# Performance work log

Hardware: AMD Instinct MI355X
Metric: run time of the kernel (lower is better)

Reference implementation:

```python
import jax, jax.numpy as jnp
import numpy as np

D = 256; H = 8; DH = D // H; FF = 1024; L = 2048; M = 1024


def _mlp(x, w0, b0, w1, b1, w2, b2):
    # 3-layer MLP, relu on all but last (matches MLP class)
    x = jax.nn.relu(x @ w0 + b0)
    x = jax.nn.relu(x @ w1 + b1)
    return x @ w2 + b2


def _ln(x, g, b, eps=1e-5):
    m = jnp.mean(x, axis=-1, keepdims=True)
    v = jnp.var(x, axis=-1, keepdims=True)
    return (x - m) * jax.lax.rsqrt(v + eps) * g + b


def setup_inputs():
    key = jax.random.key(0)
    ks = jax.random.split(key, 16)
    p = lambda i, shape: jax.random.normal(ks[i], shape, jnp.float32) * 0.02
    z = lambda *s: jnp.zeros(s, jnp.float32)
    o = lambda *s: jnp.ones(s, jnp.float32)
    # positions: ego covers [0, L), agent covers [L-M, 2L-M) -> exactly M shared positions
    return {
        'ego_q': jax.random.normal(ks[0], (1, L, D), jnp.float32),
        'agent_q': jax.random.normal(ks[1], (1, L, D), jnp.float32),
        'ego_pos': jnp.arange(L, dtype=jnp.int32),
        'agent_pos': jnp.arange(L, dtype=jnp.int32) + (L - M),
        'n_match': M,
        'fw0': p(2, (2 * D, D)), 'fb0': z(D),
        'fw1': p(3, (D, D)), 'fb1': z(D),
        'fw2': p(4, (D, D)), 'fb2': z(D),
        'wq': p(5, (D, D)), 'bq': z(D),
        'wk': p(6, (D, D)), 'bk': z(D),
        'wv': p(7, (D, D)), 'bv': z(D),
        'wo': p(8, (D, D)), 'bo': z(D),
        'g1': o(D), 'be1': z(D),
        'l1w': p(9, (D, FF)), 'l1b': z(FF),
        'l2w': p(10, (FF, D)), 'l2b': z(D),
        'g2': o(D), 'be2': z(D),
    }


def reference(ego_q, agent_q, ego_pos, agent_pos, n_match,
              fw0, fb0, fw1, fb1, fw2, fb2,
              wq, bq, wk, bk, wv, bv, wo, bo,
              g1, be1, l1w, l1b, l2w, l2b, g2, be2):
    La = agent_pos.shape[0]
    # vectorized replacement of the per-position dict/loop grouping:
    # for each ego position, find a matching agent position (positions sorted+unique)
    idx = jnp.clip(jnp.searchsorted(agent_pos, ego_pos), 0, La - 1)
    matched = (agent_pos[idx] == ego_pos)                     # (L,)
    pair = jnp.concatenate([ego_q, agent_q[:, idx, :]], axis=-1)  # (1, L, 2D)
    fused = _mlp(pair, fw0, fb0, fw1, fb1, fw2, fb2)          # (1, L, D)
    ego_out = jnp.where(matched[None, :, None], fused, ego_q)
    # agent queries whose positions are NOT in ego's set: indices [n_match, La)
    q = jnp.concatenate([ego_out, agent_q[:, n_match:, :]], axis=1)  # (1, 2L-M, D)
    kv = jnp.concatenate([ego_q, agent_q], axis=1)                   # (1, 2L, D)
    # MultiheadAttention (batch_first, eval mode -> no dropout)
    qh = (q @ wq + bq).reshape(1, -1, H, DH)
    kh = (kv @ wk + bk).reshape(1, -1, H, DH)
    vh = (kv @ wv + bv).reshape(1, -1, H, DH)
    scores = jnp.einsum('bqhd,bkhd->bhqk', qh, kh) * (1.0 / np.sqrt(DH))
    attn = jax.nn.softmax(scores, axis=-1)
    o = jnp.einsum('bhqk,bkhd->bqhd', attn, vh).reshape(1, -1, D) @ wo + bo
    x = _ln(q + o, g1, be1)
    ff = jax.nn.relu(x @ l1w + l1b) @ l2w + l2b
    return _ln(x + ff, g2, be2)
```

## Files before the change

kernel.cpp:

```cpp
#include <hip/hip_runtime.h>
#include <hip/hip_bf16.h>

typedef __hip_bfloat16 bf16;
typedef __bf16 bf16x8 __attribute__((ext_vector_type(8)));
typedef float  f32x16 __attribute__((ext_vector_type(16)));

__device__ __forceinline__ bool is_bf16_flag(const unsigned* g1w) {
    return *g1w == 0x3F803F80u;
}

__device__ __forceinline__ unsigned cvt_pk_bf16(float lo, float hi) {
    unsigned w;
    asm("v_cvt_pk_bf16_f32 %0, %1, %2" : "=v"(w) : "v"(lo), "v"(hi));
    return w;
}
__device__ __forceinline__ void permlane32_swap(unsigned& a, unsigned& b) {
    asm("v_permlane32_swap_b32 %0, %1" : "+v"(a), "+v"(b));
}

union FragU { unsigned u[4]; uint4 q; bf16x8 v; };

__device__ __forceinline__ float loadf(const void* p, size_t i, bool isb) {
    return isb ? __bfloat162float(((const bf16*)p)[i]) : ((const float*)p)[i];
}

__device__ __forceinline__ float4 load4rt(const void* p, size_t i, bool isb) {
    if (isb) {
        uint2 u = *(const uint2*)((const bf16*)p + i);
        float4 f;
        f.x = __uint_as_float(u.x << 16);
        f.y = __uint_as_float(u.x & 0xFFFF0000u);
        f.z = __uint_as_float(u.y << 16);
        f.w = __uint_as_float(u.y & 0xFFFF0000u);
        return f;
    }
    return *(const float4*)((const float*)p + i);
}

__device__ __forceinline__ void store4b(bf16* p, float4 v) {
    uint2 w;
    w.x = cvt_pk_bf16(v.x, v.y);
    w.y = cvt_pk_bf16(v.z, v.w);
    *(uint2*)p = w;
}

__device__ __forceinline__ float4 load4b(const bf16* p) {
    uint2 u = *(const uint2*)p;
    float4 f;
    f.x = __uint_as_float(u.x << 16);
    f.y = __uint_as_float(u.x & 0xFFFF0000u);
    f.z = __uint_as_float(u.y << 16);
    f.w = __uint_as_float(u.y & 0xFFFF0000u);
    return f;
}

#define NCVT 13
struct CvtArgs {
    const void* src[NCVT];
    float*      dst[NCVT];
    float       scale[NCVT];
    int         n4[NCVT];
    int         blk_end[NCVT];
};

__global__ void convert_all_kernel(CvtArgs a, const unsigned* __restrict__ g1w) {
    bool isb = is_bf16_flag(g1w);
    int b = blockIdx.x;
    int t = 0;
    while (b >= a.blk_end[t]) t++;
    int base = (t == 0) ? 0 : a.blk_end[t - 1];
    int i = (b - base) * 256 + threadIdx.x;
    if (i >= a.n4[t]) return;
    float sc = a.scale[t];
    float4 r = load4rt(a.src[t], (size_t)i * 4, isb);
    r.x *= sc; r.y *= sc; r.z *= sc; r.w *= sc;
    ((float4*)a.dst[t])[i] = r;
}

#define NWT 9
struct WtArgs {
    const void* src[NWT];
    bf16*       dst[NWT];
    int         K[NWT];
    int         N[NWT];
    float       scale[NWT];
    int         blk_end[NWT];
};

__global__ void wtrans_kernel(WtArgs a, const unsigned* __restrict__ g1w) {
    bool isb = is_bf16_flag(g1w);
    int b = blockIdx.x;
    int w = 0;
    while (b >= a.blk_end[w]) w++;
    int base = (w == 0) ? 0 : a.blk_end[w - 1];
    int tt = b - base;
    int tn = a.N[w] >> 6;
    int kr = (tt / tn) * 64, nc = (tt % tn) * 64;
    int N = a.N[w], K = a.K[w];
    float sc = a.scale[w];
    const void* src = a.src[w];
    __shared__ float ld[64][65];
    int t = threadIdx.x;
#pragma unroll
    for (int i = 0; i < 16; i++) {
        int f = t + i * 256;
        int r = f >> 6, c = f & 63;
        ld[r][c] = loadf(src, (size_t)(kr + r) * N + nc + c, isb) * sc;
    }
    __syncthreads();
    bf16* dst = a.dst[w];
#pragma unroll
    for (int i = 0; i < 16; i++) {
        int f = t + i * 256;
        int c = f >> 6, r = f & 63;
        dst[(size_t)(nc + c) * K + kr + r] = __float2bfloat16(ld[r][c]);
    }
}

__global__ void build_pair_kernel(const void* __restrict__ ego, const void* __restrict__ agent,
                                  const int* __restrict__ epos, const int* __restrict__ apos,
                                  int La, bf16* __restrict__ pair, int* __restrict__ mflag,
                                  const unsigned* __restrict__ g1w) {
    bool isb = is_bf16_flag(g1w);
    int t = threadIdx.x;
    int rb = t >> 7;
    int row = blockIdx.x * 2 + rb;
    int cc = (t & 127) * 4;
    __shared__ int s_idx[2];
    if ((t & 127) == 0) {
        int p = epos[row];
        int lo = 0, hi = La;
        while (lo < hi) { int mid = (lo + hi) >> 1; if (apos[mid] < p) lo = mid + 1; else hi = mid; }
        int idx = lo < La - 1 ? lo : La - 1;
        s_idx[rb] = idx;
        mflag[row] = (apos[idx] == p) ? 1 : 0;
    }
    __syncthreads();
    int idx = s_idx[rb];
    float4 v = (cc < 256) ? load4rt(ego, (size_t)row * 256 + cc, isb)
                          : load4rt(agent, (size_t)idx * 256 + (cc - 256), isb);
    store4b(pair + (size_t)row * 512 + cc, v);
}

template<int RELU>
__launch_bounds__(256)
__global__ void gemm_bf16_kernel(const bf16* __restrict__ A, const bf16* __restrict__ Bt,
                                 const float* __restrict__ bias, bf16* __restrict__ C,
                                 int M, int N, int K, int lda, int ldb, int ldc) {
    __shared__ __align__(16) char sA[64 * 128];
    __shared__ __align__(16) char sB[64 * 128];
    const int z = blockIdx.z;
    A += (size_t)z * K;
    Bt += (size_t)z * K;
    C += (size_t)z * M * ldc;

    const int t = threadIdx.x;
    const int lane = t & 63, wave = t >> 6;
    const int hi = lane >> 5, ql = lane & 31;
    const int bm = blockIdx.y * 64, bn = blockIdx.x * 64;
    const int wm = (wave & 1) * 32, wn = (wave >> 1) * 32;

    const int r0 = t >> 3, ch0 = t & 7;
    const int r1 = 32 + r0;
    const int wb0 = (r0 * 128 + ch0 * 16) ^ ((r0 & 7) << 4);
    const int wb1 = (r1 * 128 + ch0 * 16) ^ ((r1 & 7) << 4);

    uint4 ra0, ra1, rb0, rb1;
    {
        ra0 = *(const uint4*)&A [(size_t)(bm + r0) * lda + ch0 * 8];
        ra1 = *(const uint4*)&A [(size_t)(bm + r1) * lda + ch0 * 8];
        rb0 = *(const uint4*)&Bt[(size_t)(bn + r0) * ldb + ch0 * 8];
        rb1 = *(const uint4*)&Bt[(size_t)(bn + r1) * ldb + ch0 * 8];
    }

    f32x16 acc = {};
    const int swzA = ((wm + ql) & 7) << 4;
    const int swzB = ((wn + ql) & 7) << 4;
    const int rowA = (wm + ql) * 128;
    const int rowB = (wn + ql) * 128;

    for (int k0 = 0; k0 < K; k0 += 64) {
        __syncthreads();
        *(uint4*)(sA + wb0) = ra0;
        *(uint4*)(sA + wb1) = ra1;
        *(uint4*)(sB + wb0) = rb0;
        *(uint4*)(sB + wb1) = rb1;
        if (k0 + 64 < K) {
            int kn = k0 + 64;
            ra0 = *(const uint4*)&A [(size_t)(bm + r0) * lda + kn + ch0 * 8];
            ra1 = *(const uint4*)&A [(size_t)(bm + r1) * lda + kn + ch0 * 8];
            rb0 = *(const uint4*)&Bt[(size_t)(bn + r0) * ldb + kn + ch0 * 8];
            rb1 = *(const uint4*)&Bt[(size_t)(bn + r1) * ldb + kn + ch0 * 8];
        }
        __syncthreads();
#pragma unroll
        for (int kc = 0; kc < 4; kc++) {
            FragU af, bf_;
            af.q  = *(const uint4*)(sA + ((rowA + kc * 32 + hi * 16) ^ swzA));
            bf_.q = *(const uint4*)(sB + ((rowB + kc * 32 + hi * 16) ^ swzB));
            acc = __builtin_amdgcn_mfma_f32_32x32x16_bf16(af.v, bf_.v, acc, 0, 0, 0);
        }
    }

    int gn = bn + wn + ql;
    float bsv = (z == 0) ? bias[gn] : 0.f;
#pragma unroll
    for (int r = 0; r < 16; r++) {
        int mrow = (r & 3) + 8 * (r >> 2) + 4 * hi;
        float v = acc[r] + bsv;
        if (RELU) v = fmaxf(v, 0.f);
        C[(size_t)(bm + wm + mrow) * ldc + gn] = __float2bfloat16(v);
    }
}

__global__ void build_qkv_kernel(const void* __restrict__ ego, const void* __restrict__ agent,
                                 const bf16* __restrict__ fused, const int* __restrict__ mflag,
                                 int L, int Mm, int Nq, int Nk,
                                 bf16* __restrict__ qb, bf16* __restrict__ kvb,
                                 const unsigned* __restrict__ g1w) {
    bool isb = is_bf16_flag(g1w);
    int wave = threadIdx.x >> 6, lane = threadIdx.x & 63;
    int r = blockIdx.x * 4 + wave;
    int col = lane * 4;
    float4 kvv = (r < L) ? load4rt(ego, (size_t)r * 256 + col, isb)
                         : load4rt(agent, (size_t)(r - L) * 256 + col, isb);
    store4b(kvb + (size_t)r * 256 + col, kvv);
    if (r < Nq) {
        float4 qv;
        if (r < L) qv = mflag[r] ? load4b(fused + (size_t)r * 256 + col)
                                 : load4rt(ego, (size_t)r * 256 + col, isb);
        else       qv = load4rt(agent, (size_t)(Mm + r - L) * 256 + col, isb);
        store4b(qb + (size_t)r * 256 + col, qv);
    }
}

#define SPLITS 4

__launch_bounds__(256)
__global__ void attn_mfma_kernel(const bf16* __restrict__ qh,
                                 const bf16* __restrict__ kvh,
                                 float* __restrict__ pm, float* __restrict__ pl,
                                 bf16* __restrict__ pacc,
                                 int Nq, int Nk) {
    __shared__ __align__(16) char sK[64 * 128];
    __shared__ __align__(16) char sV[32 * 128];

    const int h = blockIdx.y, z = blockIdx.z;
    const int t = threadIdx.x;
    const int wave = t >> 6, lane = t & 63;
    const int ql = lane & 31, hi = lane >> 5;
    const int qbase = blockIdx.x * 128 + wave * 32;
    const int kbeg = z * (Nk / SPLITS);
    const int nkk = Nk / SPLITS;

    FragU qf0, qf1;
    {
        const bf16* qp = qh + (size_t)(qbase + ql) * 256 + h * 32;
        qf0.q = *(const uint4*)(qp + hi * 8);
        qf1.q = *(const uint4*)(qp + 16 + hi * 8);
    }

    float mrun = -1e30f, lrun = 0.f;
    f32x16 acc = {};

    const int skey = t >> 2, sch = t & 3;
    const int kwb = (skey * 128 + sch * 16) ^ ((skey & 7) << 4);

    uint4 rk = *(const uint4*)(kvh + (size_t)(kbeg + skey) * 512 + h * 32 + sch * 8);
    uint4 rv = *(const uint4*)(kvh + (size_t)(kbeg + lane) * 512 + 256 + h * 32 + wave * 8);

#pragma unroll 1
    for (int t0 = 0; t0 < nkk; t0 += 64) {
        __syncthreads();
        *(uint4*)(sK + kwb) = rk;
        {
            unsigned short sv[8] = {
                (unsigned short)(rv.x), (unsigned short)(rv.x >> 16),
                (unsigned short)(rv.y), (unsigned short)(rv.y >> 16),
                (unsigned short)(rv.z), (unsigned short)(rv.z >> 16),
                (unsigned short)(rv.w), (unsigned short)(rv.w >> 16)};
#pragma unroll
            for (int i = 0; i < 8; i++) {
                int dh = wave * 8 + i;
                *(unsigned short*)(sV + dh * 128 + ((lane * 2) ^ (i << 4))) = sv[i];
            }
        }
        if (t0 + 64 < nkk) {
            rk = *(const uint4*)(kvh + (size_t)(kbeg + t0 + 64 + skey) * 512 + h * 32 + sch * 8);
            rv = *(const uint4*)(kvh + (size_t)(kbeg + t0 + 64 + lane) * 512 + 256 + h * 32 + wave * 8);
        }
        __syncthreads();

        FragU ka, kb;
        f32x16 s0 = {}, s1 = {};
        {
            int row0 = ql, row1 = 32 + ql;
            int swz = (ql & 7) << 4;
            ka.q = *(const uint4*)(sK + ((row0 * 128 + hi * 16) ^ swz));
            s0 = __builtin_amdgcn_mfma_f32_32x32x16_bf16(ka.v, qf0.v, s0, 0, 0, 0);
            ka.q = *(const uint4*)(sK + ((row0 * 128 + 32 + hi * 16) ^ swz));
            s0 = __builtin_amdgcn_mfma_f32_32x32x16_bf16(ka.v, qf1.v, s0, 0, 0, 0);
            kb.q = *(const uint4*)(sK + ((row1 * 128 + hi * 16) ^ swz));
            s1 = __builtin_amdgcn_mfma_f32_32x32x16_bf16(kb.v, qf0.v, s1, 0, 0, 0);
            kb.q = *(const uint4*)(sK + ((row1 * 128 + 32 + hi * 16) ^ swz));
            s1 = __builtin_amdgcn_mfma_f32_32x32x16_bf16(kb.v, qf1.v, s1, 0, 0, 0);
        }

        float tm = -1e30f;
#pragma unroll
        for (int r = 0; r < 16; r++) tm = fmaxf(tm, fmaxf(s0[r], s1[r]));
        tm = fmaxf(tm, __shfl_xor(tm, 32));
        if (!__all(tm <= mrun)) {
            float mn = fmaxf(mrun, tm);
            float cf = __builtin_amdgcn_exp2f(mrun - mn);
            mrun = mn;
#pragma unroll
            for (int r = 0; r < 16; r++) acc[r] *= cf;
            lrun *= cf;
        }

        float p0[16], p1[16];
        float ls = 0.f;
#pragma unroll
        for (int r = 0; r < 16; r++) { p0[r] = __builtin_amdgcn_exp2f(s0[r] - mrun); ls += p0[r]; }
#pragma unroll
        for (int r = 0; r < 16; r++) { p1[r] = __builtin_amdgcn_exp2f(s1[r] - mrun); ls += p1[r]; }
        ls += __shfl_xor(ls, 32);
        lrun += ls;

        int swz = (ql & 7) << 4;
        FragU vf, pa;
        {
            unsigned a = cvt_pk_bf16(p0[0], p0[1]),  b = cvt_pk_bf16(p0[2], p0[3]);
            unsigned c = cvt_pk_bf16(p0[4], p0[5]),  d = cvt_pk_bf16(p0[6], p0[7]);
            permlane32_swap(a, c); permlane32_swap(b, d);
            pa.u[0] = a; pa.u[1] = b; pa.u[2] = c; pa.u[3] = d;
            vf.q = *(const uint4*)(sV + ((ql * 128 + hi * 16) ^ swz));
            acc = __builtin_amdgcn_mfma_f32_32x32x16_bf16(vf.v, pa.v, acc, 0, 0, 0);
            unsigned e = cvt_pk_bf16(p0[8], p0[9]),   f = cvt_pk_bf16(p0[10], p0[11]);
            unsigned g = cvt_pk_bf16(p0[12], p0[13]), h2 = cvt_pk_bf16(p0[14], p0[15]);
            permlane32_swap(e, g); permlane32_swap(f, h2);
            pa.u[0] = e; pa.u[1] = f; pa.u[2] = g; pa.u[3] = h2;
            vf.q = *(const uint4*)(sV + ((ql * 128 + 32 + hi * 16) ^ swz));
            acc = __builtin_amdgcn_mfma_f32_32x32x16_bf16(vf.v, pa.v, acc, 0, 0, 0);
        }
        {
            unsigned a = cvt_pk_bf16(p1[0], p1[1]),  b = cvt_pk_bf16(p1[2], p1[3]);
            unsigned c = cvt_pk_bf16(p1[4], p1[5]),  d = cvt_pk_bf16(p1[6], p1[7]);
            permlane32_swap(a, c); permlane32_swap(b, d);
            pa.u[0] = a; pa.u[1] = b; pa.u[2] = c; pa.u[3] = d;
            vf.q = *(const uint4*)(sV + ((ql * 128 + 64 + hi * 16) ^ swz));
            acc = __builtin_amdgcn_mfma_f32_32x32x16_bf16(vf.v, pa.v, acc, 0, 0, 0);
            unsigned e = cvt_pk_bf16(p1[8], p1[9]),   f = cvt_pk_bf16(p1[10], p1[11]);
            unsigned g = cvt_pk_bf16(p1[12], p1[13]), h2 = cvt_pk_bf16(p1[14], p1[15]);
            permlane32_swap(e, g); permlane32_swap(f, h2);
            pa.u[0] = e; pa.u[1] = f; pa.u[2] = g; pa.u[3] = h2;
            vf.q = *(const uint4*)(sV + ((ql * 128 + 96 + hi * 16) ^ swz));
            acc = __builtin_amdgcn_mfma_f32_32x32x16_bf16(vf.v, pa.v, acc, 0, 0, 0);
        }
    }

    if (hi == 0) {
        pm[((size_t)z * 8 + h) * Nq + qbase + ql] = mrun;
        pl[((size_t)z * 8 + h) * Nq + qbase + ql] = lrun;
    }
#pragma unroll
    for (int r = 0; r < 16; r++) {
        int dh = (r & 3) + 8 * (r >> 2) + 4 * hi;
        pacc[(((size_t)z * 8 + h) * 32 + dh) * (size_t)Nq + qbase + ql] = __float2bfloat16(acc[r]);
    }
}

__global__ void attn_merge_kernel(const float* __restrict__ pm, const float* __restrict__ pl,
                                  const bf16* __restrict__ pacc, bf16* __restrict__ o, int Nq) {
    int q = blockIdx.x * 256 + threadIdx.x;
    int h = blockIdx.y, dg = blockIdx.z;
    float ml[SPLITS];
    float M = -1e30f;
#pragma unroll
    for (int s = 0; s < SPLITS; s++) {
        ml[s] = pm[((size_t)s * 8 + h) * Nq + q];
        M = fmaxf(M, ml[s]);
    }
    float L = 0.f;
    float w[SPLITS];
#pragma unroll
    for (int s = 0; s < SPLITS; s++) {
        w[s] = __builtin_amdgcn_exp2f(ml[s] - M);
        L += pl[((size_t)s * 8 + h) * Nq + q] * w[s];
    }
    float inv = 1.f / L;
#pragma unroll
    for (int j = 0; j < 4; j++) {
        int d = dg * 4 + j;
        float a = 0.f;
#pragma unroll
        for (int s = 0; s < SPLITS; s++)
            a += __bfloat162float(pacc[(((size_t)s * 8 + h) * 32 + d) * (size_t)Nq + q]) * w[s];
        o[(size_t)q * 256 + h * 32 + d] = __float2bfloat16(a * inv);
    }
}

__global__ void ln_kernel(const bf16* __restrict__ a, const bf16* __restrict__ b,
                          const bf16* __restrict__ c,
                          const float* __restrict__ g, const float* __restrict__ be,
                          bf16* __restrict__ outf16, void* __restrict__ outb,
                          const unsigned* __restrict__ g1w) {
    int wave = threadIdx.x >> 6, lane = threadIdx.x & 63;
    int row = blockIdx.x * 4 + wave;
    int col = lane * 4;
    size_t base = (size_t)row * 256 + col;
    float4 av = load4b(a + base);
    float4 bv = load4b(b + base);
    float x0 = av.x + bv.x, x1 = av.y + bv.y, x2 = av.z + bv.z, x3 = av.w + bv.w;
    if (c) {
        float4 cv = load4b(c + base);
        x0 += cv.x; x1 += cv.y; x2 += cv.z; x3 += cv.w;
    }
    float s  = x0 + x1 + x2 + x3;
    float s2 = x0 * x0 + x1 * x1 + x2 * x2 + x3 * x3;
#pragma unroll
    for (int off = 32; off; off >>= 1) { s += __shfl_xor(s, off); s2 += __shfl_xor(s2, off); }
    float mean = s * (1.f / 256.f);
    float var  = s2 * (1.f / 256.f) - mean * mean;
    float rs = rsqrtf(var + 1e-5f);
    float4 gv = *(const float4*)(g + col);
    float4 bev = *(const float4*)(be + col);
    float y0 = (x0 - mean) * rs * gv.x + bev.x;
    float y1 = (x1 - mean) * rs * gv.y + bev.y;
    float y2 = (x2 - mean) * rs * gv.z + bev.z;
    float y3 = (x3 - mean) * rs * gv.w + bev.w;
    if (outf16) {
        store4b(outf16 + base, make_float4(y0, y1, y2, y3));
    } else if (is_bf16_flag(g1w)) {
        store4b((bf16*)outb + base, make_float4(y0, y1, y2, y3));
    } else {
        *(float4*)((float*)outb + base) = make_float4(y0, y1, y2, y3);
    }
}

extern "C" void kernel_launch(void* const* d_in, const int* in_sizes, int n_in,
                              void* d_out, int out_size, void* d_ws, size_t ws_size,
                              hipStream_t stream) {
    const int Dd = 256;
    const int L  = in_sizes[2];
    const int La = in_sizes[3];
    const int Nk = L + La;
    const int Nq = out_size / Dd;
    const int Mm = L + La - Nq;
    const float scale = 0.17677669529663687f * 1.4426950408889634f;

    const unsigned* g1w = (const unsigned*)d_in[19];

    float* W = (float*)d_ws;
    size_t off = 0;
    auto alloc = [&](size_t n) { size_t o = off; off += n; return o; };
    (void)ws_size; (void)n_in;

    size_t o_fb0 = alloc(256), o_fb1 = alloc(256), o_fb2 = alloc(256);
    size_t o_bq = alloc(256), o_bkv = alloc(512), o_bo = alloc(256);
    size_t o_g1 = alloc(256), o_be1 = alloc(256);
    size_t o_l1b = alloc(1024), o_l2b = alloc(256);
    size_t o_g2 = alloc(256), o_be2 = alloc(256);

    size_t o_fw0t = alloc(65536), o_fw1t = alloc(32768), o_fw2t = alloc(32768);
    size_t o_wqt = alloc(32768), o_wkvt = alloc(65536), o_wot = alloc(32768);
    size_t o_l1wt = alloc(131072), o_l2wt = alloc(131072);
    size_t o_pair = alloc((size_t)L * 256);
    size_t o_h1 = alloc((size_t)L * 128), o_h2 = alloc((size_t)L * 128);
    size_t o_fused = alloc((size_t)L * 128);
    size_t o_q   = alloc((size_t)Nq * 128);
    size_t o_kv  = alloc((size_t)Nk * 128);
    size_t o_qh  = alloc((size_t)Nq * 128);
    size_t o_kvh = alloc((size_t)Nk * 256);
    size_t o_ao  = alloc((size_t)Nq * 128);
    size_t o_opp = alloc((size_t)Nq * 256);
    size_t o_x   = alloc((size_t)Nq * 128);
    size_t o_ff1 = alloc((size_t)Nq * 512);
    size_t o_ff2p = alloc((size_t)Nq * 256);
    size_t o_pacc = alloc((size_t)SPLITS * 8 * 16 * Nq);
    size_t o_pm   = alloc((size_t)SPLITS * 8 * Nq);
    size_t o_pl   = alloc((size_t)SPLITS * 8 * Nq);
    size_t o_ints = alloc((size_t)L);
    int* mflag = (int*)(W + o_ints);

    auto B16 = [&](size_t o) { return (bf16*)(W + o); };

    {
        CvtArgs ca;
        const int srcs[NCVT] = {6, 8, 10, 12, 14, 16, 18, 19, 20, 22, 24, 25, 26};
        const size_t dsts[NCVT] = {o_fb0, o_fb1, o_fb2, o_bq, o_bkv, o_bkv + 256, o_bo,
                                   o_g1, o_be1, o_l1b, o_l2b, o_g2, o_be2};
        int blk = 0;
        for (int i = 0; i < NCVT; i++) {
            ca.src[i] = d_in[srcs[i]];
            ca.dst[i] = W + dsts[i];
            ca.scale[i] = (srcs[i] == 12) ? scale : 1.0f;
            ca.n4[i] = in_sizes[srcs[i]] / 4;
            blk += (ca.n4[i] + 255) / 256;
            ca.blk_end[i] = blk;
        }
        convert_all_kernel<<<blk, 256, 0, stream>>>(ca, g1w);
    }

    {
        WtArgs wa;
        const int srcs[NWT] = {5, 7, 9, 11, 13, 15, 17, 21, 23};
        bf16* dsts[NWT] = {B16(o_fw0t), B16(o_fw1t), B16(o_fw2t), B16(o_wqt),
                           B16(o_wkvt), B16(o_wkvt) + 65536, B16(o_wot),
                           B16(o_l1wt), B16(o_l2wt)};
        const int Ks[NWT] = {512, 256, 256, 256, 256, 256, 256, 256, 1024};
        const int Ns[NWT] = {256, 256, 256, 256, 256, 256, 256, 1024, 256};
        int blk = 0;
        for (int i = 0; i < NWT; i++) {
            wa.src[i] = d_in[srcs[i]];
            wa.dst[i] = dsts[i];
            wa.K[i] = Ks[i]; wa.N[i] = Ns[i];
            wa.scale[i] = (srcs[i] == 11) ? scale : 1.0f;
            blk += (Ks[i] / 64) * (Ns[i] / 64);
            wa.blk_end[i] = blk;
        }
        wtrans_kernel<<<blk, 256, 0, stream>>>(wa, g1w);
    }

    build_pair_kernel<<<L / 2, 256, 0, stream>>>(d_in[0], d_in[1],
                                                 (const int*)d_in[2], (const int*)d_in[3],
                                                 La, B16(o_pair), mflag, g1w);

    gemm_bf16_kernel<1><<<dim3(4, L/64), 256, 0, stream>>>(B16(o_pair), B16(o_fw0t), W + o_fb0, B16(o_h1),    L, 256, 512, 512, 512, 256);
    gemm_bf16_kernel<1><<<dim3(4, L/64), 256, 0, stream>>>(B16(o_h1),   B16(o_fw1t), W + o_fb1, B16(o_h2),    L, 256, 256, 256, 256, 256);
    gemm_bf16_kernel<0><<<dim3(4, L/64), 256, 0, stream>>>(B16(o_h2),   B16(o_fw2t), W + o_fb2, B16(o_fused), L, 256, 256, 256, 256, 256);

    build_qkv_kernel<<<Nk / 4, 256, 0, stream>>>(d_in[0], d_in[1], B16(o_fused), mflag,
                                                 L, Mm, Nq, Nk, B16(o_q), B16(o_kv), g1w);

    gemm_bf16_kernel<0><<<dim3(4, Nq/64), 256, 0, stream>>>(B16(o_q),  B16(o_wqt),  W + o_bq,  B16(o_qh),  Nq, 256, 256, 256, 256, 256);
    gemm_bf16_kernel<0><<<dim3(8, Nk/64), 256, 0, stream>>>(B16(o_kv), B16(o_wkvt), W + o_bkv, B16(o_kvh), Nk, 512, 256, 256, 256, 512);

    attn_mfma_kernel<<<dim3(Nq/128, 8, SPLITS), 256, 0, stream>>>(B16(o_qh), B16(o_kvh),
                                                                  W + o_pm, W + o_pl, B16(o_pacc),
                                                                  Nq, Nk);
    attn_merge_kernel<<<dim3(Nq/256, 8, 8), 256, 0, stream>>>(W + o_pm, W + o_pl, B16(o_pacc),
                                                              B16(o_ao), Nq);

    gemm_bf16_kernel<0><<<dim3(4, Nq/64, 2), 256, 0, stream>>>(B16(o_ao), B16(o_wot), W + o_bo, B16(o_opp), Nq, 256, 128, 256, 256, 256);
    ln_kernel<<<Nq / 4, 256, 0, stream>>>(B16(o_q), B16(o_opp), B16(o_opp) + (size_t)Nq * 256,
                                          W + o_g1, W + o_be1, B16(o_x), nullptr, g1w);

    gemm_bf16_kernel<1><<<dim3(16, Nq/64), 256, 0, stream>>>(B16(o_x),   B16(o_l1wt), W + o_l1b, B16(o_ff1), Nq, 1024, 256, 256, 256, 1024);
    gemm_bf16_kernel<0><<<dim3(4,  Nq/64, 2), 256, 0, stream>>>(B16(o_ff1), B16(o_l2wt), W + o_l2b, B16(o_ff2p), Nq, 256, 512, 1024, 1024, 256);
    ln_kernel<<<Nq / 4, 256, 0, stream>>>(B16(o_x), B16(o_ff2p), B16(o_ff2p) + (size_t)Nq * 256,
                                          W + o_g2, W + o_be2, nullptr, d_out, g1w);
}
```

Before: 107.7 us.

## Fuse preprocessing kernels, merge Q/KV projection GEMMs, and raise attention splits

```diff
diff --git a/kernel.cpp b/kernel.cpp
--- a/kernel.cpp
+++ b/kernel.cpp
@@ -55,109 +55,99 @@
 }
 
 #define NCVT 13
-struct CvtArgs {
-    const void* src[NCVT];
-    float*      dst[NCVT];
-    float       scale[NCVT];
-    int         n4[NCVT];
-    int         blk_end[NCVT];
+#define NWT 9
+struct PreArgs {
+    const void* csrc[NCVT];
+    float*      cdst[NCVT];
+    float       cscale[NCVT];
+    int         cn4[NCVT];
+    int         cblk_end[NCVT];
+    int         cvt_blocks;
+    const void* wsrc[NWT];
+    bf16*       wdst[NWT];
+    int         wK[NWT];
+    int         wN[NWT];
+    float       wscale[NWT];
+    int         wblk_end[NWT];
+    int         wt_blocks;
+    const void* ego; const void* agent;
+    const int*  epos; const int* apos;
+    int         La;
+    bf16*       pair;
+    int*        mflag;
 };
 
-__global__ void convert_all_kernel(CvtArgs a, const unsigned* __restrict__ g1w) {
+__global__ void preprocess_kernel(PreArgs a, const unsigned* __restrict__ g1w) {
     bool isb = is_bf16_flag(g1w);
+    __shared__ float ld[64][65];
+    __shared__ int s_idx[2];
     int b = blockIdx.x;
-    int t = 0;
-    while (b >= a.blk_end[t]) t++;
-    int base = (t == 0) ? 0 : a.blk_end[t - 1];
-    int i = (b - base) * 256 + threadIdx.x;
-    if (i >= a.n4[t]) return;
-    float sc = a.scale[t];
-    float4 r = load4rt(a.src[t], (size_t)i * 4, isb);
-    r.x *= sc; r.y *= sc; r.z *= sc; r.w *= sc;
-    ((float4*)a.dst[t])[i] = r;
-}
-
-#define NWT 9
-struct WtArgs {
-    const void* src[NWT];
-    bf16*       dst[NWT];
-    int         K[NWT];
-    int         N[NWT];
-    float       scale[NWT];
-    int         blk_end[NWT];
-};
-
-__global__ void wtrans_kernel(WtArgs a, const unsigned* __restrict__ g1w) {
-    bool isb = is_bf16_flag(g1w);
-    int b = blockIdx.x;
-    int w = 0;
-    while (b >= a.blk_end[w]) w++;
-    int base = (w == 0) ? 0 : a.blk_end[w - 1];
-    int tt = b - base;
-    int tn = a.N[w] >> 6;
-    int kr = (tt / tn) * 64, nc = (tt % tn) * 64;
-    int N = a.N[w], K = a.K[w];
-    float sc = a.scale[w];
-    const void* src = a.src[w];
-    __shared__ float ld[64][65];
-    int t = threadIdx.x;
-#pragma unroll
-    for (int i = 0; i < 16; i++) {
-        int f = t + i * 256;
-        int r = f >> 6, c = f & 63;
-        ld[r][c] = loadf(src, (size_t)(kr + r) * N + nc + c, isb) * sc;
-    }
-    __syncthreads();
-    bf16* dst = a.dst[w];
-#pragma unroll
-    for (int i = 0; i < 16; i++) {
-        int f = t + i * 256;
-        int c = f >> 6, r = f & 63;
-        dst[(size_t)(nc + c) * K + kr + r] = __float2bfloat16(ld[r][c]);
-    }
-}
-
-__global__ void build_pair_kernel(const void* __restrict__ ego, const void* __restrict__ agent,
-                                  const int* __restrict__ epos, const int* __restrict__ apos,
-                                  int La, bf16* __restrict__ pair, int* __restrict__ mflag,
-                                  const unsigned* __restrict__ g1w) {
-    bool isb = is_bf16_flag(g1w);
-    int t = threadIdx.x;
-    int rb = t >> 7;
-    int row = blockIdx.x * 2 + rb;
-    int cc = (t & 127) * 4;
-    __shared__ int s_idx[2];
-    if ((t & 127) == 0) {
-        int p = epos[row];
-        int lo = 0, hi = La;
-        while (lo < hi) { int mid = (lo + hi) >> 1; if (apos[mid] < p) lo = mid + 1; else hi = mid; }
-        int idx = lo < La - 1 ? lo : La - 1;
-        s_idx[rb] = idx;
-        mflag[row] = (apos[idx] == p) ? 1 : 0;
-    }
-    __syncthreads();
-    int idx = s_idx[rb];
-    float4 v = (cc < 256) ? load4rt(ego, (size_t)row * 256 + cc, isb)
-                          : load4rt(agent, (size_t)idx * 256 + (cc - 256), isb);
-    store4b(pair + (size_t)row * 512 + cc, v);
+    int tid = threadIdx.x;
+    if (b < a.cvt_blocks) {
+        int t = 0;
+        while (b >= a.cblk_end[t]) t++;
+        int base = (t == 0) ? 0 : a.cblk_end[t - 1];
+        int i = (b - base) * 256 + tid;
+        if (i >= a.cn4[t]) return;
+        float sc = a.cscale[t];
+        float4 r = load4rt(a.csrc[t], (size_t)i * 4, isb);
+        r.x *= sc; r.y *= sc; r.z *= sc; r.w *= sc;
+        ((float4*)a.cdst[t])[i] = r;
+    } else if (b < a.cvt_blocks + a.wt_blocks) {
+        b -= a.cvt_blocks;
+        int w = 0;
+        while (b >= a.wblk_end[w]) w++;
+        int base = (w == 0) ? 0 : a.wblk_end[w - 1];
+        int tt = b - base;
+        int tn = a.wN[w] >> 6;
+        int kr = (tt / tn) * 64, nc = (tt % tn) * 64;
+        int N = a.wN[w], K = a.wK[w];
+        float sc = a.wscale[w];
+        const void* src = a.wsrc[w];
+#pragma unroll
+        for (int i = 0; i < 16; i++) {
+            int f = tid + i * 256;
+            int r = f >> 6, c = f & 63;
+            ld[r][c] = loadf(src, (size_t)(kr + r) * N + nc + c, isb) * sc;
+        }
+        __syncthreads();
+        bf16* dst = a.wdst[w];
+#pragma unroll
+        for (int i = 0; i < 16; i++) {
+            int f = tid + i * 256;
+            int c = f >> 6, r = f & 63;
+            dst[(size_t)(nc + c) * K + kr + r] = __float2bfloat16(ld[r][c]);
+        }
+    } else {
+        b -= a.cvt_blocks + a.wt_blocks;
+        int rb = tid >> 7;
+        int row = b * 2 + rb;
+        int cc = (tid & 127) * 4;
+        if ((tid & 127) == 0) {
+            int p = a.epos[row];
+            int lo = 0, hi = a.La;
+            while (lo < hi) { int mid = (lo + hi) >> 1; if (a.apos[mid] < p) lo = mid + 1; else hi = mid; }
+            int idx = lo < a.La - 1 ? lo : a.La - 1;
+            s_idx[rb] = idx;
+            a.mflag[row] = (a.apos[idx] == p) ? 1 : 0;
+        }
+        __syncthreads();
+        int idx = s_idx[rb];
+        float4 v = (cc < 256) ? load4rt(a.ego, (size_t)row * 256 + cc, isb)
+                              : load4rt(a.agent, (size_t)idx * 256 + (cc - 256), isb);
+        store4b(a.pair + (size_t)row * 512 + cc, v);
+    }
 }
 
 template<int RELU>
-__launch_bounds__(256)
-__global__ void gemm_bf16_kernel(const bf16* __restrict__ A, const bf16* __restrict__ Bt,
-                                 const float* __restrict__ bias, bf16* __restrict__ C,
-                                 int M, int N, int K, int lda, int ldb, int ldc) {
-    __shared__ __align__(16) char sA[64 * 128];
-    __shared__ __align__(16) char sB[64 * 128];
-    const int z = blockIdx.z;
-    A += (size_t)z * K;
-    Bt += (size_t)z * K;
-    C += (size_t)z * M * ldc;
-
+__device__ __forceinline__ void gemm_core(const bf16* __restrict__ A, const bf16* __restrict__ Bt,
+                                          const float* __restrict__ bias, bf16* __restrict__ C,
+                                          int K, int lda, int ldb, int ldc,
+                                          int bm, int bn, bool addBias,
+                                          char* sA, char* sB) {
     const int t = threadIdx.x;
     const int lane = t & 63, wave = t >> 6;
     const int hi = lane >> 5, ql = lane & 31;
-    const int bm = blockIdx.y * 64, bn = blockIdx.x * 64;
     const int wm = (wave & 1) * 32, wn = (wave >> 1) * 32;
 
     const int r0 = t >> 3, ch0 = t & 7;
@@ -203,7 +193,7 @@
     }
 
     int gn = bn + wn + ql;
-    float bsv = (z == 0) ? bias[gn] : 0.f;
+    float bsv = addBias ? bias[gn] : 0.f;
 #pragma unroll
     for (int r = 0; r < 16; r++) {
         int mrow = (r & 3) + 8 * (r >> 2) + 4 * hi;
@@ -211,6 +201,34 @@
         if (RELU) v = fmaxf(v, 0.f);
         C[(size_t)(bm + wm + mrow) * ldc + gn] = __float2bfloat16(v);
     }
+}
+
+template<int RELU>
+__launch_bounds__(256)
+__global__ void gemm_bf16_kernel(const bf16* __restrict__ A, const bf16* __restrict__ Bt,
+                                 const float* __restrict__ bias, bf16* __restrict__ C,
+                                 int M, int N, int K, int lda, int ldb, int ldc) {
+    __shared__ __align__(16) char sA[64 * 128];
+    __shared__ __align__(16) char sB[64 * 128];
+    const int z = blockIdx.z;
+    gemm_core<RELU>(A + (size_t)z * K, Bt + (size_t)z * K, bias, C + (size_t)z * M * ldc,
+                    K, lda, ldb, ldc, blockIdx.y * 64, blockIdx.x * 64, z == 0, sA, sB);
+}
+
+struct GemmP {
+    const bf16* A; const bf16* Bt; const float* bias; bf16* C;
+    int K, lda, ldb, ldc, nx;
+};
+
+__launch_bounds__(256)
+__global__ void gemm_dual_kernel(GemmP p0, GemmP p1, int nblk0) {
+    __shared__ __align__(16) char sA[64 * 128];
+    __shared__ __align__(16) char sB[64 * 128];
+    int b = blockIdx.x;
+    const GemmP& p = (b < nblk0) ? p0 : p1;
+    int t = (b < nblk0) ? b : b - nblk0;
+    int bn = (t % p.nx) * 64, bm = (t / p.nx) * 64;
+    gemm_core<0>(p.A, p.Bt, p.bias, p.C, p.K, p.lda, p.ldb, p.ldc, bm, bn, true, sA, sB);
 }
 
 __global__ void build_qkv_kernel(const void* __restrict__ ego, const void* __restrict__ agent,
@@ -234,7 +252,7 @@
     }
 }
 
-#define SPLITS 4
+#define SPLITS 8
 
 __launch_bounds__(256)
 __global__ void attn_mfma_kernel(const bf16* __restrict__ qh,
@@ -487,45 +505,45 @@
     auto B16 = [&](size_t o) { return (bf16*)(W + o); };
 
     {
-        CvtArgs ca;
-        const int srcs[NCVT] = {6, 8, 10, 12, 14, 16, 18, 19, 20, 22, 24, 25, 26};
-        const size_t dsts[NCVT] = {o_fb0, o_fb1, o_fb2, o_bq, o_bkv, o_bkv + 256, o_bo,
-                                   o_g1, o_be1, o_l1b, o_l2b, o_g2, o_be2};
+        PreArgs pa;
+        const int csrcs[NCVT] = {6, 8, 10, 12, 14, 16, 18, 19, 20, 22, 24, 25, 26};
+        const size_t cdsts[NCVT] = {o_fb0, o_fb1, o_fb2, o_bq, o_bkv, o_bkv + 256, o_bo,
+                                    o_g1, o_be1, o_l1b, o_l2b, o_g2, o_be2};
         int blk = 0;
         for (int i = 0; i < NCVT; i++) {
-            ca.src[i] = d_in[srcs[i]];
-            ca.dst[i] = W + dsts[i];
-            ca.scale[i] = (srcs[i] == 12) ? scale : 1.0f;
-            ca.n4[i] = in_sizes[srcs[i]] / 4;
-            blk += (ca.n4[i] + 255) / 256;
-            ca.blk_end[i] = blk;
-        }
-        convert_all_kernel<<<blk, 256, 0, stream>>>(ca, g1w);
-    }
-
-    {
-        WtArgs wa;
-        const int srcs[NWT] = {5, 7, 9, 11, 13, 15, 17, 21, 23};
-        bf16* dsts[NWT] = {B16(o_fw0t), B16(o_fw1t), B16(o_fw2t), B16(o_wqt),
-                           B16(o_wkvt), B16(o_wkvt) + 65536, B16(o_wot),
-                           B16(o_l1wt), B16(o_l2wt)};
+            pa.csrc[i] = d_in[csrcs[i]];
+            pa.cdst[i] = W + cdsts[i];
+            pa.cscale[i] = (csrcs[i] == 12) ? scale : 1.0f;
+            pa.cn4[i] = in_sizes[csrcs[i]] / 4;
+            blk += (pa.cn4[i] + 255) / 256;
+            pa.cblk_end[i] = blk;
+        }
+        pa.cvt_blocks = blk;
+
+        const int wsrcs[NWT] = {5, 7, 9, 11, 13, 15, 17, 21, 23};
+        bf16* wdsts[NWT] = {B16(o_fw0t), B16(o_fw1t), B16(o_fw2t), B16(o_wqt),
+                            B16(o_wkvt), B16(o_wkvt) + 65536, B16(o_wot),
+                            B16(o_l1wt), B16(o_l2wt)};
         const int Ks[NWT] = {512, 256, 256, 256, 256, 256, 256, 256, 1024};
         const int Ns[NWT] = {256, 256, 256, 256, 256, 256, 256, 1024, 256};
-        int blk = 0;
+        int wblk = 0;
         for (int i = 0; i < NWT; i++) {
-            wa.src[i] = d_in[srcs[i]];
-            wa.dst[i] = dsts[i];
-            wa.K[i] = Ks[i]; wa.N[i] = Ns[i];
-            wa.scale[i] = (srcs[i] == 11) ? scale : 1.0f;
-            blk += (Ks[i] / 64) * (Ns[i] / 64);
-            wa.blk_end[i] = blk;
-        }
-        wtrans_kernel<<<blk, 256, 0, stream>>>(wa, g1w);
-    }
-
-    build_pair_kernel<<<L / 2, 256, 0, stream>>>(d_in[0], d_in[1],
-                                                 (const int*)d_in[2], (const int*)d_in[3],
-                                                 La, B16(o_pair), mflag, g1w);
+            pa.wsrc[i] = d_in[wsrcs[i]];
+            pa.wdst[i] = wdsts[i];
+            pa.wK[i] = Ks[i]; pa.wN[i] = Ns[i];
+            pa.wscale[i] = (wsrcs[i] == 11) ? scale : 1.0f;
+            wblk += (Ks[i] / 64) * (Ns[i] / 64);
+            pa.wblk_end[i] = wblk;
+        }
+        pa.wt_blocks = wblk;
+
+        pa.ego = d_in[0]; pa.agent = d_in[1];
+        pa.epos = (const int*)d_in[2]; pa.apos = (const int*)d_in[3];
+        pa.La = La; pa.pair = B16(o_pair); pa.mflag = mflag;
+
+        int total = pa.cvt_blocks + pa.wt_blocks + L / 2;
+        preprocess_kernel<<<total, 256, 0, stream>>>(pa, g1w);
+    }
 
     gemm_bf16_kernel<1><<<dim3(4, L/64), 256, 0, stream>>>(B16(o_pair), B16(o_fw0t), W + o_fb0, B16(o_h1),    L, 256, 512, 512, 512, 256);
     gemm_bf16_kernel<1><<<dim3(4, L/64), 256, 0, stream>>>(B16(o_h1),   B16(o_fw1t), W + o_fb1, B16(o_h2),    L, 256, 256, 256, 256, 256);
@@ -534,8 +552,13 @@
     build_qkv_kernel<<<Nk / 4, 256, 0, stream>>>(d_in[0], d_in[1], B16(o_fused), mflag,
                                                  L, Mm, Nq, Nk, B16(o_q), B16(o_kv), g1w);
 
-    gemm_bf16_kernel<0><<<dim3(4, Nq/64), 256, 0, stream>>>(B16(o_q),  B16(o_wqt),  W + o_bq,  B16(o_qh),  Nq, 256, 256, 256, 256, 256);
-    gemm_bf16_kernel<0><<<dim3(8, Nk/64), 256, 0, stream>>>(B16(o_kv), B16(o_wkvt), W + o_bkv, B16(o_kvh), Nk, 512, 256, 256, 256, 512);
+    {
+        GemmP p0{B16(o_q),  B16(o_wqt),  W + o_bq,  B16(o_qh),  256, 256, 256, 256, 4};
+        GemmP p1{B16(o_kv), B16(o_wkvt), W + o_bkv, B16(o_kvh), 256, 256, 256, 512, 8};
+        int nblk0 = 4 * (Nq / 64);
+        int nblk1 = 8 * (Nk / 64);
+        gemm_dual_kernel<<<nblk0 + nblk1, 256, 0, stream>>>(p0, p1, nblk0);
+    }
 
     attn_mfma_kernel<<<dim3(Nq/128, 8, SPLITS), 256, 0, stream>>>(B16(o_qh), B16(o_kvh),
                                                                   W + o_pm, W + o_pl, B16(o_pacc),
```

After: 97.48 us. 9.5% less time.
